# Performance work log

Measured on AMD Instinct MI355X. Metric: run time of the kernel, lower is better.

## Reference

```python
import jax, jax.numpy as jnp
import numpy as np

B, C_IN, H, W = 64, 32, 28, 28
K = 5                       # receptive field
OH, OW = H - K + 1, W - K + 1  # 24, 24 (padding=0, stride=1)
C_OUT = 128
IN_SIZE = C_IN * K * K      # 800


def setup_inputs() -> dict:
    key = jax.random.key(0)
    ks = jax.random.split(key, 7)
    x = jax.random.uniform(ks[0], (B, C_IN, H, W), dtype=jnp.float32)
    # per-output-channel tree params: layer sizes 36 -> 6 -> 1, 6 inputs/node, 64-entry LUTs
    map1 = jax.random.randint(ks[1], (C_OUT, 36, 6), 0, IN_SIZE, dtype=jnp.int32)
    lut1 = jax.random.uniform(ks[2], (C_OUT, 36, 64), dtype=jnp.float32)
    map2 = jax.random.randint(ks[3], (C_OUT, 6, 6), 0, 36, dtype=jnp.int32)
    lut2 = jax.random.uniform(ks[4], (C_OUT, 6, 64), dtype=jnp.float32)
    map3 = jax.random.randint(ks[5], (C_OUT, 1, 6), 0, 6, dtype=jnp.int32)
    lut3 = jax.random.uniform(ks[6], (C_OUT, 1, 64), dtype=jnp.float32)
    return {"x": x, "map1": map1, "lut1": lut1, "map2": map2,
            "lut2": lut2, "map3": map3, "lut3": lut3}


def _lut_eval(xin, lut):
    # xin: [P, N, 6] soft bits in [0,1]; lut: [N, 64] LUT entries.
    # out[p,n] = sum_a lut[n,a] * prod_j (x_j if bit_j(a) else 1-x_j)
    P, N, k = xin.shape
    p = jnp.ones((P, N, 1), xin.dtype)
    for j in range(k):  # build address probabilities incrementally; peak [P,N,64]
        xj = xin[:, :, j]
        pair = jnp.stack([1.0 - xj, xj], axis=-1)          # [P,N,2]
        p = (p[:, :, :, None] * pair[:, :, None, :]).reshape(P, N, -1)
    return jnp.einsum('pna,na->pn', p, lut)


def _unfold(x):
    # im2col, kernel 5, stride 1, no padding -> [B*OH*OW, C_IN*K*K]
    patches = jax.lax.conv_general_dilated_patches(
        x, (K, K), (1, 1), 'VALID')                        # [B, C*K*K, OH, OW]
    patches = patches.transpose(0, 2, 3, 1).reshape(-1, IN_SIZE)
    return patches


def _forward(x, map1, lut1, map2, lut2, map3, lut3):
    patches = _unfold(x)                                   # [P, 800]

    def tree(_, params):  # one output channel's LUT tree (chunked in torch code)
        m1, l1, m2, l2, m3, l3 = params
        h = jnp.clip(_lut_eval(patches[:, m1], l1), 0.0, 1.0)  # [P,36]
        h = jnp.clip(_lut_eval(h[:, m2], l2), 0.0, 1.0)        # [P,6]
        h = jnp.clip(_lut_eval(h[:, m3], l3), 0.0, 1.0)        # [P,1]
        return None, h[:, 0]

    _, outs = jax.lax.scan(tree, None, (map1, lut1, map2, lut2, map3, lut3))
    # outs: [C_OUT, P] -> [B, C_OUT, OH, OW]
    out = outs.T.reshape(B, OH * OW, C_OUT).transpose(0, 2, 1)
    return out.reshape(B, C_OUT, OH, OW)


def reference(x, map1, lut1, map2, lut2, map3, lut3):
    return _forward(x, map1, lut1, map2, lut2, map3, lut3)
```

## Files before the change

kernel.cpp:

```cpp
#include <hip/hip_runtime.h>

#define B_      64
#define CIN     32
#define H_      28
#define W_      28
#define OH_     24
#define OW_     24
#define COUT    128
#define NPOS    (OH_ * OW_)
#define HW_     (H_ * W_)
#define XSTRIDE (CIN * HW_)
#define PSTRIDE (CIN * HW_)

#define BLK      192
#define NQ       16
#define NLANES   (NQ * NPOS)
#define UB       (NLANES / BLK)
#define TPB      2
#define TG       (COUT / TPB)
#define NXCD     8
#define UPX      (UB / NXCD)

#define XP_BYTES   (32 * PSTRIDE * 8)
#define OFF_BYTES  (COUT * 36 * 6 * 4)
#define COEF_BYTES (COUT * 43 * 64 * 4)
#define WS_NEW     (XP_BYTES + OFF_BYTES + COEF_BYTES)

#define BLOCK    256
#define BHALF    32
#define NLANES6  (BHALF * NPOS)
#define UBLOCKS6 (NLANES6 / BLOCK)
#define TPB6     2
#define NTP      64
#define TGROUPS6 (NTP / TPB6)
#define UPX6     (UBLOCKS6 / NXCD)
#define CF4_PER_TP (43 * 32)
#define OFF6_INTS  (NTP * 36 * 12)
#define WS_R6      ((OFF6_INTS + NTP * 43 * 128) * 4)

typedef float f2 __attribute__((ext_vector_type(2)));
typedef float f4 __attribute__((ext_vector_type(4)));
struct p2 { f2 a, b; };

__device__ __forceinline__ f2 pkfma(f2 x, f2 h, f2 l) {
    return __builtin_elementwise_fma(x, h, l);
}

__device__ __forceinline__ f2 clamp2(f2 v) {
    f2 r;
    r.x = __builtin_amdgcn_fmed3f(v.x, 0.0f, 1.0f);
    r.y = __builtin_amdgcn_fmed3f(v.y, 0.0f, 1.0f);
    return r;
}

template<int I>
__device__ __forceinline__ f2 sp(f4 q) {
    return __builtin_shufflevector(q, q, I, I);
}

template<int M>
struct RecT {
    static __device__ __forceinline__ p2 go(const float* __restrict__ C, int a0,
                                            const p2* xs) {
        p2 lo = RecT<M - 1>::go(C, a0, xs);
        p2 hi = RecT<M - 1>::go(C, a0 + (1 << (M - 2)), xs);
        p2 r;
        r.a = pkfma(xs[6 - M].a, hi.a, lo.a);
        r.b = pkfma(xs[6 - M].b, hi.b, lo.b);
        return r;
    }
};
template<>
struct RecT<2> {
    static __device__ __forceinline__ p2 go(const float* __restrict__ C, int a0,
                                            const p2* xs) {
        f4 q = *(const f4*)(C + 2 * a0);
        p2 v0, v1, r;
        v0.a = pkfma(xs[5].a, sp<1>(q), sp<0>(q));
        v0.b = pkfma(xs[5].b, sp<1>(q), sp<0>(q));
        v1.a = pkfma(xs[5].a, sp<3>(q), sp<2>(q));
        v1.b = pkfma(xs[5].b, sp<3>(q), sp<2>(q));
        r.a = pkfma(xs[4].a, v1.a, v0.a);
        r.b = pkfma(xs[4].b, v1.b, v0.b);
        return r;
    }
};

__device__ __forceinline__ p2 contractT(const float* __restrict__ C, const p2 xs[6]) {
    p2 r = RecT<6>::go(C, 0, xs);
    r.a = clamp2(r.a);
    r.b = clamp2(r.b);
    return r;
}

__global__ __launch_bounds__(BLK, 3)
void lutconv_x(const char* __restrict__ xpc,
               const int* __restrict__ OFFS,
               const float* __restrict__ COEF,
               float* __restrict__ out) {
    __shared__ float CLs[TPB * 43 * 64];

    const int bid = blockIdx.x;
    const int xcd = bid % NXCD;
    const int j   = bid / NXCD;
    const int tg  = j % TG;
    const int usl = j / TG;
    const int us  = xcd * UPX + usl;

    const int g   = us * BLK + threadIdx.x;
    const int bq  = g / NPOS;
    const int pos = g - bq * NPOS;
    const int oh  = pos / OW_;
    const int ow  = pos - oh * OW_;
    const unsigned lin   = oh * W_ + ow;
    const unsigned byteA = (bq * PSTRIDE + lin) * 8u;
    const unsigned byteB = ((bq + 16) * PSTRIDE + lin) * 8u;

    {
        const f4* src = (const f4*)(COEF + (size_t)tg * (TPB * 43 * 64));
        f4* dst = (f4*)CLs;
#pragma unroll
        for (int k = 0; k < 8; ++k) {
            int i = k * BLK + threadIdx.x;
            if (i < TPB * 43 * 16) dst[i] = src[i];
        }
    }
    __syncthreads();

#pragma unroll 1
    for (int tt = 0; tt < TPB; ++tt) {
        const int t = tg * TPB + tt;
        const float* Ct = CLs + tt * (43 * 64);
        const int* Ot = OFFS + t * (36 * 6);

        p2 h2[6];
#pragma unroll
        for (int j3 = 0; j3 < 6; ++j3) {
            p2 h1[6];
#pragma unroll
            for (int j1 = 0; j1 < 6; ++j1) {
                const int* oi = Ot + (j3 * 6 + j1) * 6;
                p2 xs[6];
#pragma unroll
                for (int jj = 0; jj < 6; ++jj) {
                    int o = __builtin_amdgcn_readfirstlane(oi[jj]);
                    const char* p = xpc + o;
                    p2 w;
                    w.a = *(const f2*)(p + byteA);
                    w.b = *(const f2*)(p + byteB);
                    xs[jj] = w;
                }
                h1[j1] = contractT(Ct + (j3 * 7 + j1) * 64, xs);
            }
            h2[j3] = contractT(Ct + (j3 * 7 + 6) * 64, h1);
        }
        p2 r = contractT(Ct + 42 * 64, h2);

        const size_t istr = (size_t)16 * COUT * NPOS;
        size_t o0 = ((size_t)bq * COUT + t) * NPOS + pos;
        out[o0]            = r.a.x;
        out[o0 + 2 * istr] = r.a.y;
        out[o0 + istr]     = r.b.x;
        out[o0 + 3 * istr] = r.b.y;
    }
}

__global__ void prep_xp(const float* __restrict__ x, f2* __restrict__ xp) {
    int i = blockIdx.x * 256 + threadIdx.x;
    if (i < 32 * PSTRIDE) {
        int p = i / PSTRIDE;
        int r = i - p * PSTRIDE;
        f2 v;
        v.x = x[p * XSTRIDE + r];
        v.y = x[(p + 32) * XSTRIDE + r];
        xp[i] = v;
    }
}

__global__ void prep_cf(const int* __restrict__ map1, const float* __restrict__ lut1,
                        const int* __restrict__ map2, const float* __restrict__ lut2,
                        const int* __restrict__ map3, const float* __restrict__ lut3,
                        int* __restrict__ OFFS, float* __restrict__ COEF) {
    const int rec  = blockIdx.x % 43;
    const int t    = blockIdx.x / 43;
    const int lane = threadIdx.x;

    const float* lp;
    int node;
    if (rec == 42) {
        node = 42;
        lp = lut3 + t * 64;
    } else {
        const int j3 = rec / 7;
        const int jr = rec - 7 * j3;
        const int n2 = map3[t * 6 + j3];
        if (jr == 6) {
            node = j3 * 7 + 6;
            lp = lut2 + (t * 6 + n2) * 64;
        } else {
            const int n1 = map2[(t * 6 + n2) * 6 + jr];
            node = j3 * 7 + jr;
            lp = lut1 + (t * 36 + n1) * 64;
            if (lane < 6) {
                int m  = map1[(t * 36 + n1) * 6 + lane];
                int c  = m / 25;
                int r  = m - 25 * c;
                int kh = r / 5;
                int kw = r - 5 * kh;
                OFFS[t * 216 + (j3 * 6 + jr) * 6 + lane] =
                    (c * HW_ + kh * W_ + kw) * 8;
            }
        }
    }

    float cv = lp[lane];
#pragma unroll
    for (int s = 1; s < 64; s <<= 1) {
        float o = __shfl_xor(cv, s);
        if (lane & s) cv -= o;
    }
    COEF[((size_t)t * 43 + node) * 64 + lane] = cv;
}

template<int M>
struct RecL {
    static __device__ __forceinline__ p2 go(const f4* __restrict__ C, int a0,
                                            const p2* xs) {
        p2 lo = RecL<M - 1>::go(C, a0, xs);
        p2 hi = RecL<M - 1>::go(C, a0 + (1 << (M - 2)), xs);
        p2 r;
        r.a = pkfma(xs[6 - M].a, hi.a, lo.a);
        r.b = pkfma(xs[6 - M].b, hi.b, lo.b);
        return r;
    }
};
template<>
struct RecL<1> {
    static __device__ __forceinline__ p2 go(const f4* __restrict__ C, int a0,
                                            const p2* xs) {
        f4 q = C[a0];
        f2 lo; lo.x = q.x; lo.y = q.y;
        f2 hi; hi.x = q.z; hi.y = q.w;
        p2 r;
        r.a = pkfma(xs[5].a, hi, lo);
        r.b = pkfma(xs[5].b, hi, lo);
        return r;
    }
};

__device__ __forceinline__ p2 contract2(const f4* __restrict__ C, const p2 xs[6]) {
    p2 r = RecL<6>::go(C, 0, xs);
    r.a = clamp2(r.a);
    r.b = clamp2(r.b);
    return r;
}

__global__ __launch_bounds__(BLOCK, 3)
void lutconv_l(const float* __restrict__ x,
               const int* __restrict__ OFFS,
               const f4* __restrict__ COEF,
               float* __restrict__ out) {
    __shared__ f4 CLs[CF4_PER_TP];

    const int bid = blockIdx.x;
    const int xcd = bid % NXCD;
    const int j   = bid / NXCD;
    const int tg  = j % TGROUPS6;
    const int us  = j / TGROUPS6;
    const int u   = xcd * UPX6 + us;

    const int g   = u * BLOCK + threadIdx.x;
    const int b0  = g / NPOS;
    const int pos = g - b0 * NPOS;
    const int oh  = pos / OW_;
    const int ow  = pos - oh * OW_;
    const unsigned lin   = oh * W_ + ow;
    const unsigned voff0 = (b0 * XSTRIDE + lin) * 4u;
    const unsigned voff1 = voff0 + BHALF * XSTRIDE * 4u;
    const char* xc = (const char*)x;

#pragma unroll 1
    for (int tpi = 0; tpi < TPB6; ++tpi) {
        const int tp = tg * TPB6 + tpi;

        if (tpi) __syncthreads();
        {
            const f4* src = COEF + (size_t)tp * CF4_PER_TP;
#pragma unroll
            for (int k = 0; k < 6; ++k) {
                int i = k * BLOCK + threadIdx.x;
                if (i < CF4_PER_TP) CLs[i] = src[i];
            }
        }
        __syncthreads();

        const int* Ot = OFFS + tp * (36 * 12);

        p2 h2[6];
#pragma unroll
        for (int j3 = 0; j3 < 6; ++j3) {
            p2 h1[6];
#pragma unroll
            for (int j1 = 0; j1 < 6; ++j1) {
                const int* oi = Ot + (j3 * 6 + j1) * 12;
                p2 xs[6];
#pragma unroll
                for (int jj = 0; jj < 6; ++jj) {
                    int o0 = __builtin_amdgcn_readfirstlane(oi[2 * jj]);
                    int o1 = __builtin_amdgcn_readfirstlane(oi[2 * jj + 1]);
                    f2 va, vb;
                    va.x = *(const float*)(xc + o0 + voff0);
                    va.y = *(const float*)(xc + o1 + voff0);
                    vb.x = *(const float*)(xc + o0 + voff1);
                    vb.y = *(const float*)(xc + o1 + voff1);
                    xs[jj].a = va;
                    xs[jj].b = vb;
                }
                h1[j1] = contract2(&CLs[(j3 * 7 + j1) * 32], xs);
            }
            h2[j3] = contract2(&CLs[(j3 * 7 + 6) * 32], h1);
        }
        p2 r = contract2(&CLs[42 * 32], h2);

        size_t ob = ((size_t)b0 * COUT + 2 * tp) * NPOS + pos;
        out[ob]        = r.a.x;
        out[ob + NPOS] = r.a.y;
        size_t ob2 = ob + (size_t)BHALF * COUT * NPOS;
        out[ob2]        = r.b.x;
        out[ob2 + NPOS] = r.b.y;
    }
}

__global__ void prep_l(const int* __restrict__ map1, const float* __restrict__ lut1,
                       const int* __restrict__ map2, const float* __restrict__ lut2,
                       const int* __restrict__ map3, const float* __restrict__ lut3,
                       int* __restrict__ OFFS, float* __restrict__ COEF) {
    const int rec  = blockIdx.x % 43;
    const int tp   = blockIdx.x / 43;
    const int lane = threadIdx.x;
    const int t0 = 2 * tp, t1 = 2 * tp + 1;

    const float* lp0;
    const float* lp1;
    int node;
    if (rec == 42) {
        node = 42;
        lp0 = lut3 + t0 * 64;
        lp1 = lut3 + t1 * 64;
    } else {
        const int j3 = rec / 7;
        const int jr = rec - 7 * j3;
        const int n20 = map3[t0 * 6 + j3];
        const int n21 = map3[t1 * 6 + j3];
        if (jr == 6) {
            node = j3 * 7 + 6;
            lp0 = lut2 + (t0 * 6 + n20) * 64;
            lp1 = lut2 + (t1 * 6 + n21) * 64;
        } else {
            const int n10 = map2[(t0 * 6 + n20) * 6 + jr];
            const int n11 = map2[(t1 * 6 + n21) * 6 + jr];
            node = j3 * 7 + jr;
            lp0 = lut1 + (t0 * 36 + n10) * 64;
            lp1 = lut1 + (t1 * 36 + n11) * 64;
            if (lane < 12) {
                int h  = lane & 1;
                int jj = lane >> 1;
                int n1 = h ? n11 : n10;
                int t  = h ? t1 : t0;
                int m  = map1[(t * 36 + n1) * 6 + jj];
                int c  = m / 25;
                int r  = m - 25 * c;
                int kh = r / 5;
                int kw = r - 5 * kh;
                OFFS[(tp * 36 + j3 * 6 + jr) * 12 + jj * 2 + h] =
                    (c * HW_ + kh * W_ + kw) * 4;
            }
        }
    }

    float c0 = lp0[lane];
    float c1 = lp1[lane];
#pragma unroll
    for (int s = 1; s < 64; s <<= 1) {
        float o0 = __shfl_xor(c0, s);
        float o1 = __shfl_xor(c1, s);
        if (lane & s) { c0 -= o0; c1 -= o1; }
    }
    float* cp = COEF + ((size_t)tp * 43 + node) * 128;
    int slot = (lane >> 1) * 4 + (lane & 1) * 2;
    cp[slot]     = c0;
    cp[slot + 1] = c1;
}

__device__ __forceinline__ float clamp01(float v) {
    return __builtin_amdgcn_fmed3f(v, 0.0f, 1.0f);
}

__device__ __forceinline__ float contract64s(const float* __restrict__ L,
                                             const float xs[6]) {
    float v[32];
#pragma unroll
    for (int a = 0; a < 32; ++a) {
        float b = L[2 * a];
        v[a] = fmaf(xs[5], L[2 * a + 1] - b, b);
    }
#pragma unroll
    for (int a = 0; a < 16; ++a) v[a] = fmaf(xs[4], v[2*a+1] - v[2*a], v[2*a]);
#pragma unroll
    for (int a = 0; a < 8; ++a)  v[a] = fmaf(xs[3], v[2*a+1] - v[2*a], v[2*a]);
#pragma unroll
    for (int a = 0; a < 4; ++a)  v[a] = fmaf(xs[2], v[2*a+1] - v[2*a], v[2*a]);
#pragma unroll
    for (int a = 0; a < 2; ++a)  v[a] = fmaf(xs[1], v[2*a+1] - v[2*a], v[2*a]);
    return clamp01(fmaf(xs[0], v[1] - v[0], v[0]));
}

__global__ __launch_bounds__(BLOCK, 4)
void lutconv_fb(const float* __restrict__ x,
                const int* __restrict__ map1, const float* __restrict__ lut1,
                const int* __restrict__ map2, const float* __restrict__ lut2,
                const int* __restrict__ map3, const float* __restrict__ lut3,
                float* __restrict__ out) {
    const int g   = (blockIdx.x % 144) * BLOCK + threadIdx.x;
    const int tg  = blockIdx.x / 144;
    const int b   = g / NPOS;
    const int pos = g - b * NPOS;
    const int lin = (pos / OW_) * W_ + (pos - (pos / OW_) * OW_);
    const float* xb = x + (size_t)b * XSTRIDE;

#pragma unroll 1
    for (int tt = 0; tt < 8; ++tt) {
        const int t = tg * 8 + tt;
        float h2[6];
#pragma unroll
        for (int j3 = 0; j3 < 6; ++j3) {
            int n2 = __builtin_amdgcn_readfirstlane(map3[t * 6 + j3]);
            float h1[6];
#pragma unroll
            for (int j1 = 0; j1 < 6; ++j1) {
                int n1 = __builtin_amdgcn_readfirstlane(map2[(t * 6 + n2) * 6 + j1]);
                float xs[6];
#pragma unroll
                for (int jj = 0; jj < 6; ++jj) {
                    int m = map1[(t * 36 + n1) * 6 + jj];
                    int c = m / 25, r = m - 25 * c, kh = r / 5, kw = r - 5 * kh;
                    int off = __builtin_amdgcn_readfirstlane(c * HW_ + kh * W_ + kw);
                    xs[jj] = xb[off + lin];
                }
                h1[j1] = contract64s(lut1 + (t * 36 + n1) * 64, xs);
            }
            h2[j3] = contract64s(lut2 + (t * 6 + n2) * 64, h1);
        }
        out[((size_t)b * COUT + t) * NPOS + pos] = contract64s(lut3 + t * 64, h2);
    }
}

extern "C" void kernel_launch(void* const* d_in, const int* in_sizes, int n_in,
                              void* d_out, int out_size, void* d_ws, size_t ws_size,
                              hipStream_t stream) {
    const float* x    = (const float*)d_in[0];
    const int*   map1 = (const int*)d_in[1];
    const float* lut1 = (const float*)d_in[2];
    const int*   map2 = (const int*)d_in[3];
    const float* lut2 = (const float*)d_in[4];
    const int*   map3 = (const int*)d_in[5];
    const float* lut3 = (const float*)d_in[6];
    float* out = (float*)d_out;

    if (ws_size >= (size_t)WS_NEW) {
        f2*    xp   = (f2*)d_ws;
        int*   OFFS = (int*)((char*)d_ws + XP_BYTES);
        float* COEF = (float*)((char*)d_ws + XP_BYTES + OFF_BYTES);

        prep_xp<<<(32 * PSTRIDE + 255) / 256, 256, 0, stream>>>(x, xp);
        prep_cf<<<COUT * 43, 64, 0, stream>>>(map1, lut1, map2, lut2, map3, lut3,
                                              OFFS, COEF);
        lutconv_x<<<UB * TG, BLK, 0, stream>>>((const char*)xp, OFFS, COEF, out);
    } else if (ws_size >= (size_t)WS_R6) {
        int*   OFFS = (int*)d_ws;
        float* COEF = (float*)((char*)d_ws + OFF6_INTS * 4);
        prep_l<<<NTP * 43, 64, 0, stream>>>(map1, lut1, map2, lut2, map3, lut3,
                                            OFFS, COEF);
        lutconv_l<<<UBLOCKS6 * TGROUPS6, BLOCK, 0, stream>>>(
            x, OFFS, (const f4*)COEF, out);
    } else {
        lutconv_fb<<<144 * 16, BLOCK, 0, stream>>>(
            x, map1, lut1, map2, lut2, map3, lut3, out);
    }
}
```

Before: 460.5 us.

## Restructure LUT-tree kernel to one channel per block with fp16 LDS spill of layer-2 outputs

```diff
diff --git a/kernel.cpp b/kernel.cpp
--- a/kernel.cpp
+++ b/kernel.cpp
@@ -15,16 +15,14 @@
 #define BLK      192
 #define NQ       16
 #define NLANES   (NQ * NPOS)
-#define UB       (NLANES / BLK)
-#define TPB      2
-#define TG       (COUT / TPB)
+#define NCH      (NLANES / BLK)
 #define NXCD     8
-#define UPX      (UB / NXCD)
-
-#define XP_BYTES   (32 * PSTRIDE * 8)
-#define OFF_BYTES  (COUT * 36 * 6 * 4)
-#define COEF_BYTES (COUT * 43 * 64 * 4)
-#define WS_NEW     (XP_BYTES + OFF_BYTES + COEF_BYTES)
+#define CPX      (NCH / NXCD)
+
+#define XP_BYTES    (32 * PSTRIDE * 8)
+#define OFF_BYTES   (COUT * 36 * 6 * 4)
+#define COEF2_BYTES (COUT * 43 * 32 * 16)
+#define WS_NEW      (XP_BYTES + OFF_BYTES + COEF2_BYTES)
 
 #define BLOCK    256
 #define BHALF    32
@@ -40,6 +38,7 @@
 
 typedef float f2 __attribute__((ext_vector_type(2)));
 typedef float f4 __attribute__((ext_vector_type(4)));
+typedef __fp16 h2v __attribute__((ext_vector_type(2)));
 struct p2 { f2 a, b; };
 
 __device__ __forceinline__ f2 pkfma(f2 x, f2 h, f2 l) {
@@ -53,17 +52,12 @@
     return r;
 }
 
-template<int I>
-__device__ __forceinline__ f2 sp(f4 q) {
-    return __builtin_shufflevector(q, q, I, I);
-}
-
 template<int M>
-struct RecT {
-    static __device__ __forceinline__ p2 go(const float* __restrict__ C, int a0,
+struct RecD {
+    static __device__ __forceinline__ p2 go(const f4* __restrict__ C, int a0,
                                             const p2* xs) {
-        p2 lo = RecT<M - 1>::go(C, a0, xs);
-        p2 hi = RecT<M - 1>::go(C, a0 + (1 << (M - 2)), xs);
+        p2 lo = RecD<M - 1>::go(C, a0, xs);
+        p2 hi = RecD<M - 1>::go(C, a0 + (1 << (M - 2)), xs);
         p2 r;
         r.a = pkfma(xs[6 - M].a, hi.a, lo.a);
         r.b = pkfma(xs[6 - M].b, hi.b, lo.b);
@@ -71,41 +65,59 @@
     }
 };
 template<>
-struct RecT<2> {
-    static __device__ __forceinline__ p2 go(const float* __restrict__ C, int a0,
+struct RecD<1> {
+    static __device__ __forceinline__ p2 go(const f4* __restrict__ C, int a0,
                                             const p2* xs) {
-        f4 q = *(const f4*)(C + 2 * a0);
-        p2 v0, v1, r;
-        v0.a = pkfma(xs[5].a, sp<1>(q), sp<0>(q));
-        v0.b = pkfma(xs[5].b, sp<1>(q), sp<0>(q));
-        v1.a = pkfma(xs[5].a, sp<3>(q), sp<2>(q));
-        v1.b = pkfma(xs[5].b, sp<3>(q), sp<2>(q));
-        r.a = pkfma(xs[4].a, v1.a, v0.a);
-        r.b = pkfma(xs[4].b, v1.b, v0.b);
+        f4 q = C[a0];
+        f2 lo; lo.x = q.x; lo.y = q.y;
+        f2 hi; hi.x = q.z; hi.y = q.w;
+        p2 r;
+        r.a = pkfma(xs[5].a, hi, lo);
+        r.b = pkfma(xs[5].b, hi, lo);
         return r;
     }
 };
 
-__device__ __forceinline__ p2 contractT(const float* __restrict__ C, const p2 xs[6]) {
-    p2 r = RecT<6>::go(C, 0, xs);
+__device__ __forceinline__ p2 contractD(const f4* __restrict__ C, const p2 xs[6]) {
+    p2 r = RecD<6>::go(C, 0, xs);
     r.a = clamp2(r.a);
     r.b = clamp2(r.b);
     return r;
 }
 
-__global__ __launch_bounds__(BLK, 3)
-void lutconv_x(const char* __restrict__ xpc,
+__device__ __forceinline__ unsigned pk16(f2 v) {
+    h2v h = __builtin_amdgcn_cvt_pkrtz(v.x, v.y);
+    return __builtin_bit_cast(unsigned, h);
+}
+__device__ __forceinline__ f2 unpk16(unsigned u) {
+    h2v h = __builtin_bit_cast(h2v, u);
+    f2 r; r.x = (float)h.x; r.y = (float)h.y;
+    return r;
+}
+
+__global__ __launch_bounds__(BLK, 4)
+void lutconv_s(const char* __restrict__ xpc,
                const int* __restrict__ OFFS,
-               const float* __restrict__ COEF,
+               const f4* __restrict__ COEF,
                float* __restrict__ out) {
-    __shared__ float CLs[TPB * 43 * 64];
+    __shared__ f4 CLs[43 * 32];
+    __shared__ uint2 H2s[6][BLK];
 
     const int bid = blockIdx.x;
-    const int xcd = bid % NXCD;
-    const int j   = bid / NXCD;
-    const int tg  = j % TG;
-    const int usl = j / TG;
-    const int us  = xcd * UPX + usl;
+    const int xcd = bid & 7;
+    const int j   = bid >> 3;
+    const int t   = j & 127;
+    const int usl = j >> 7;
+    const int us  = xcd * CPX + usl;
+
+    {
+        const f4* src = COEF + (size_t)t * (43 * 32);
+#pragma unroll
+        for (int k = 0; k < 8; ++k) {
+            int i = k * BLK + threadIdx.x;
+            if (i < 43 * 32) CLs[i] = src[i];
+        }
+    }
 
     const int g   = us * BLK + threadIdx.x;
     const int bq  = g / NPOS;
@@ -115,54 +127,45 @@
     const unsigned lin   = oh * W_ + ow;
     const unsigned byteA = (bq * PSTRIDE + lin) * 8u;
     const unsigned byteB = ((bq + 16) * PSTRIDE + lin) * 8u;
-
-    {
-        const f4* src = (const f4*)(COEF + (size_t)tg * (TPB * 43 * 64));
-        f4* dst = (f4*)CLs;
-#pragma unroll
-        for (int k = 0; k < 8; ++k) {
-            int i = k * BLK + threadIdx.x;
-            if (i < TPB * 43 * 16) dst[i] = src[i];
-        }
-    }
     __syncthreads();
 
 #pragma unroll 1
-    for (int tt = 0; tt < TPB; ++tt) {
-        const int t = tg * TPB + tt;
-        const float* Ct = CLs + tt * (43 * 64);
-        const int* Ot = OFFS + t * (36 * 6);
-
-        p2 h2[6];
-#pragma unroll
-        for (int j3 = 0; j3 < 6; ++j3) {
-            p2 h1[6];
-#pragma unroll
-            for (int j1 = 0; j1 < 6; ++j1) {
-                const int* oi = Ot + (j3 * 6 + j1) * 6;
-                p2 xs[6];
-#pragma unroll
-                for (int jj = 0; jj < 6; ++jj) {
-                    int o = __builtin_amdgcn_readfirstlane(oi[jj]);
-                    const char* p = xpc + o;
-                    p2 w;
-                    w.a = *(const f2*)(p + byteA);
-                    w.b = *(const f2*)(p + byteB);
-                    xs[jj] = w;
-                }
-                h1[j1] = contractT(Ct + (j3 * 7 + j1) * 64, xs);
-            }
-            h2[j3] = contractT(Ct + (j3 * 7 + 6) * 64, h1);
-        }
-        p2 r = contractT(Ct + 42 * 64, h2);
-
-        const size_t istr = (size_t)16 * COUT * NPOS;
-        size_t o0 = ((size_t)bq * COUT + t) * NPOS + pos;
-        out[o0]            = r.a.x;
-        out[o0 + 2 * istr] = r.a.y;
-        out[o0 + istr]     = r.b.x;
-        out[o0 + 3 * istr] = r.b.y;
-    }
+    for (int j3 = 0; j3 < 6; ++j3) {
+        const int* oi3 = OFFS + t * 216 + j3 * 36;
+        p2 h1[6];
+#pragma unroll
+        for (int j1 = 0; j1 < 6; ++j1) {
+            p2 xs[6];
+#pragma unroll
+            for (int jj = 0; jj < 6; ++jj) {
+                int o = __builtin_amdgcn_readfirstlane(oi3[j1 * 6 + jj]);
+                const char* p = xpc + o;
+                p2 w;
+                w.a = *(const f2*)(p + byteA);
+                w.b = *(const f2*)(p + byteB);
+                xs[jj] = w;
+            }
+            h1[j1] = contractD(CLs + (j3 * 7 + j1) * 32, xs);
+        }
+        p2 h2 = contractD(CLs + (j3 * 7 + 6) * 32, h1);
+        H2s[j3][threadIdx.x] = make_uint2(pk16(h2.a), pk16(h2.b));
+    }
+
+    p2 xs[6];
+#pragma unroll
+    for (int j3 = 0; j3 < 6; ++j3) {
+        uint2 v = H2s[j3][threadIdx.x];
+        xs[j3].a = unpk16(v.x);
+        xs[j3].b = unpk16(v.y);
+    }
+    p2 r = contractD(CLs + 42 * 32, xs);
+
+    const size_t istr = (size_t)16 * COUT * NPOS;
+    size_t o0 = ((size_t)bq * COUT + t) * NPOS + pos;
+    out[o0]            = r.a.x;
+    out[o0 + 2 * istr] = r.a.y;
+    out[o0 + istr]     = r.b.x;
+    out[o0 + 3 * istr] = r.b.y;
 }
 
 __global__ void prep_xp(const float* __restrict__ x, f2* __restrict__ xp) {
@@ -177,10 +180,10 @@
     }
 }
 
-__global__ void prep_cf(const int* __restrict__ map1, const float* __restrict__ lut1,
-                        const int* __restrict__ map2, const float* __restrict__ lut2,
-                        const int* __restrict__ map3, const float* __restrict__ lut3,
-                        int* __restrict__ OFFS, float* __restrict__ COEF) {
+__global__ void prep_cf2(const int* __restrict__ map1, const float* __restrict__ lut1,
+                         const int* __restrict__ map2, const float* __restrict__ lut2,
+                         const int* __restrict__ map3, const float* __restrict__ lut3,
+                         int* __restrict__ OFFS, float* __restrict__ COEF) {
     const int rec  = blockIdx.x % 43;
     const int t    = blockIdx.x / 43;
     const int lane = threadIdx.x;
@@ -219,40 +222,10 @@
         float o = __shfl_xor(cv, s);
         if (lane & s) cv -= o;
     }
-    COEF[((size_t)t * 43 + node) * 64 + lane] = cv;
-}
-
-template<int M>
-struct RecL {
-    static __device__ __forceinline__ p2 go(const f4* __restrict__ C, int a0,
-                                            const p2* xs) {
-        p2 lo = RecL<M - 1>::go(C, a0, xs);
-        p2 hi = RecL<M - 1>::go(C, a0 + (1 << (M - 2)), xs);
-        p2 r;
-        r.a = pkfma(xs[6 - M].a, hi.a, lo.a);
-        r.b = pkfma(xs[6 - M].b, hi.b, lo.b);
-        return r;
-    }
-};
-template<>
-struct RecL<1> {
-    static __device__ __forceinline__ p2 go(const f4* __restrict__ C, int a0,
-                                            const p2* xs) {
-        f4 q = C[a0];
-        f2 lo; lo.x = q.x; lo.y = q.y;
-        f2 hi; hi.x = q.z; hi.y = q.w;
-        p2 r;
-        r.a = pkfma(xs[5].a, hi, lo);
-        r.b = pkfma(xs[5].b, hi, lo);
-        return r;
-    }
-};
-
-__device__ __forceinline__ p2 contract2(const f4* __restrict__ C, const p2 xs[6]) {
-    p2 r = RecL<6>::go(C, 0, xs);
-    r.a = clamp2(r.a);
-    r.b = clamp2(r.b);
-    return r;
+    float* cp = COEF + ((size_t)t * 43 + node) * 128;
+    int a = lane >> 1, h = lane & 1;
+    cp[a * 4 + h * 2]     = cv;
+    cp[a * 4 + h * 2 + 1] = cv;
 }
 
 __global__ __launch_bounds__(BLOCK, 3)
@@ -316,11 +289,11 @@
                     xs[jj].a = va;
                     xs[jj].b = vb;
                 }
-                h1[j1] = contract2(&CLs[(j3 * 7 + j1) * 32], xs);
-            }
-            h2[j3] = contract2(&CLs[(j3 * 7 + 6) * 32], h1);
-        }
-        p2 r = contract2(&CLs[42 * 32], h2);
+                h1[j1] = contractD(&CLs[(j3 * 7 + j1) * 32], xs);
+            }
+            h2[j3] = contractD(&CLs[(j3 * 7 + 6) * 32], h1);
+        }
+        p2 r = contractD(&CLs[42 * 32], h2);
 
         size_t ob = ((size_t)b0 * COUT + 2 * tp) * NPOS + pos;
         out[ob]        = r.a.x;
@@ -473,9 +446,10 @@
         float* COEF = (float*)((char*)d_ws + XP_BYTES + OFF_BYTES);
 
         prep_xp<<<(32 * PSTRIDE + 255) / 256, 256, 0, stream>>>(x, xp);
-        prep_cf<<<COUT * 43, 64, 0, stream>>>(map1, lut1, map2, lut2, map3, lut3,
-                                              OFFS, COEF);
-        lutconv_x<<<UB * TG, BLK, 0, stream>>>((const char*)xp, OFFS, COEF, out);
+        prep_cf2<<<COUT * 43, 64, 0, stream>>>(map1, lut1, map2, lut2, map3, lut3,
+                                               OFFS, COEF);
+        lutconv_s<<<NCH * COUT, BLK, 0, stream>>>((const char*)xp, OFFS,
+                                                  (const f4*)COEF, out);
     } else if (ws_size >= (size_t)WS_R6) {
         int*   OFFS = (int*)d_ws;
         float* COEF = (float*)((char*)d_ws + OFF6_INTS * 4);
```

Result: no change. 465.5 us (+1.1%).
